# Optimization experiments

Hardware: AMD Instinct MI355X
Metric: run time of the kernel (lower is better)

The kernel has to match this reference:

```python
import jax, jax.numpy as jnp
import numpy as np

EPS = 0.1

def _kernels():
    # torch: sobel = [[-0.5,0,0.5]]*3 (2D), repeated along depth -> [1,1,3,3,3]
    s = np.array([[-0.5, 0.0, 0.5]] * 3, dtype=np.float32)        # grad along W
    kx = np.tile(s[None, :, :], (3, 1, 1))                        # [3,3,3]
    ky = np.tile(s.T[None, :, :], (3, 1, 1))                      # grad along H
    kz = np.zeros((3, 3, 3), dtype=np.float32)
    kz[0, :, :] = -0.5
    kz[2, :, :] = 0.5                                             # grad along D
    # OIDHW, O=I=1 (channel=1 depthwise)
    return (jnp.asarray(kx)[None, None], jnp.asarray(ky)[None, None], jnp.asarray(kz)[None, None])

KX, KY, KZ = _kernels()

def _conv(x, k):
    return jax.lax.conv_general_dilated(
        x, k, window_strides=(1, 1, 1), padding='VALID',
        dimension_numbers=('NCDHW', 'OIDHW', 'NCDHW'))

def _grads(x):
    # ReplicationPad3d(1) == edge padding on D,H,W
    xp = jnp.pad(x, ((0, 0), (0, 0), (1, 1), (1, 1), (1, 1)), mode='edge')
    return _conv(xp, KX), _conv(xp, KY), _conv(xp, KZ)

def setup_inputs() -> dict:
    key = jax.random.key(0)
    k1, k2, k3 = jax.random.split(key, 3)
    shp = (1, 1, 192, 192, 192)
    return {
        'I': jax.random.normal(k1, shp, dtype=jnp.float32),
        'J': jax.random.normal(k2, shp, dtype=jnp.float32),
        'mask': jax.random.uniform(k3, shp, dtype=jnp.float32),
    }

def reference(I, J, mask):
    Ix, Iy, Iz = _grads(I)
    Jx, Jy, Jz = _grads(J)
    I_mag = Ix * Ix + Iy * Iy + Iz * Iz + EPS * EPS
    J_mag = Jx * Jx + Jy * Jy + Jz * Jz + EPS * EPS
    dot = Ix * Jx + Iy * Jy + Iz * Jz          # == sum over concat channel dim (C=1)
    ngf = (dot * dot) / (I_mag * J_mag)
    return jnp.mean((1.0 - ngf) * mask)
```

## Files before the change

### kernel.cpp

```cpp
#include <hip/hip_runtime.h>

#define NN 192
#define BZ 4
#define YC 12
#define NTHR (64 * BZ)


__device__ __forceinline__ void fold_pq(const float3 rm, const float3 r0, const float3 rp,
                                        int lane, float pe[5], float qe[5]) {
    const float p0 = rm.x + r0.x + rp.x;
    const float p1 = rm.y + r0.y + rp.y;
    const float p2 = rm.z + r0.z + rp.z;
    const float q0 = rp.x - rm.x;
    const float q1 = rp.y - rm.y;
    const float q2 = rp.z - rm.z;
    float pL = __shfl_up(p2, 1, 64);
    float pR = __shfl_down(p0, 1, 64);
    float qL = __shfl_up(q2, 1, 64);
    float qR = __shfl_down(q0, 1, 64);
    if (lane == 0)  { pL = p0; qL = q0; }
    if (lane == 63) { pR = p2; qR = q2; }
    pe[0] = pL; pe[1] = p0; pe[2] = p1; pe[3] = p2; pe[4] = pR;
    qe[0] = qL; qe[1] = q0; qe[2] = q1; qe[3] = q2; qe[4] = qR;
}

__device__ __forceinline__ void load_plane(const float* const base[6], int yrow,
                                           float3 rI[3], float3 rJ[3]) {
#pragma unroll
    for (int d = 0; d < 3; ++d) rI[d] = *reinterpret_cast<const float3*>(base[d] + yrow);
#pragma unroll
    for (int d = 0; d < 3; ++d) rJ[d] = *reinterpret_cast<const float3*>(base[3 + d] + yrow);
}

__global__ __launch_bounds__(NTHR, 3) void ngf_kernel(const float* __restrict__ I,
                                                      const float* __restrict__ J,
                                                      const float* __restrict__ M,
                                                      float* __restrict__ out) {
    const int lane = threadIdx.x;
    const int tz = threadIdx.y;
    const int xoff = lane * 3;
    const int z = blockIdx.y * BZ + tz;
    const int ybase = blockIdx.x * YC;

    const int gzm = (z == 0) ? 0 : z - 1;
    const int gzp = (z == NN - 1) ? (NN - 1) : z + 1;

    const float* base[6] = {
        I + gzm * NN * NN + xoff, I + z * NN * NN + xoff, I + gzp * NN * NN + xoff,
        J + gzm * NN * NN + xoff, J + z * NN * NN + xoff, J + gzp * NN * NN + xoff};
    const float* mbase = M + z * NN * NN + xoff;

    float pe[2][3][5], qe[2][3][5];

    {
        float3 rI[3], rJ[3];
        load_plane(base, ((ybase == 0) ? 0 : (ybase - 1)) * NN, rI, rJ);
        fold_pq(rI[0], rI[1], rI[2], lane, pe[0][0], qe[0][0]);
        fold_pq(rJ[0], rJ[1], rJ[2], lane, pe[1][0], qe[1][0]);
        load_plane(base, ybase * NN, rI, rJ);
        fold_pq(rI[0], rI[1], rI[2], lane, pe[0][1], qe[0][1]);
        fold_pq(rJ[0], rJ[1], rJ[2], lane, pe[1][1], qe[1][1]);
    }

    float3 bI[2][3], bJ[2][3];
    load_plane(base, (ybase + 1) * NN, bI[0], bJ[0]);
    float3 mcur = *reinterpret_cast<const float3*>(mbase + ybase * NN);

    float acc = 0.0f;
#pragma unroll
    for (int yy = 0; yy < YC; ++yy) {
        const int cb = yy & 1, nb = cb ^ 1;

        float3 mnxt = mcur;
        if (yy < YC - 1) {
            int gy = ybase + yy + 2;
            gy = (gy > NN - 1) ? (NN - 1) : gy;
            load_plane(base, gy * NN, bI[nb], bJ[nb]);
            mnxt = *reinterpret_cast<const float3*>(mbase + (ybase + yy + 1) * NN);
        }

        const int sC = (yy + 2) % 3;
        fold_pq(bI[cb][0], bI[cb][1], bI[cb][2], lane, pe[0][sC], qe[0][sC]);
        fold_pq(bJ[cb][0], bJ[cb][1], bJ[cb][2], lane, pe[1][sC], qe[1][sC]);

        const int s0 = yy % 3, s1 = (yy + 1) % 3;
        float G[2][3][3];
#pragma unroll
        for (int ar = 0; ar < 2; ++ar) {
            float S[5], D[5], T[5];
#pragma unroll
            for (int i = 0; i < 5; ++i) {
                S[i] = pe[ar][s0][i] + pe[ar][s1][i] + pe[ar][sC][i];
                D[i] = pe[ar][sC][i] - pe[ar][s0][i];
                T[i] = qe[ar][s0][i] + qe[ar][s1][i] + qe[ar][sC][i];
            }
#pragma unroll
            for (int i = 0; i < 3; ++i) {
                G[ar][0][i] = S[i + 2] - S[i];
                G[ar][1][i] = D[i] + D[i + 1] + D[i + 2];
                G[ar][2][i] = T[i] + T[i + 1] + T[i + 2];
            }
        }
        const float mm[3] = {mcur.x, mcur.y, mcur.z};
#pragma unroll
        for (int i = 0; i < 3; ++i) {
            const float Ix = G[0][0][i], Iy = G[0][1][i], Iz = G[0][2][i];
            const float Jx = G[1][0][i], Jy = G[1][1][i], Jz = G[1][2][i];
            const float im = Ix * Ix + Iy * Iy + Iz * Iz + 0.04f;
            const float jm = Jx * Jx + Jy * Jy + Jz * Jz + 0.04f;
            const float dot = Ix * Jx + Iy * Jy + Iz * Jz;
            acc += (1.0f - dot * dot * __builtin_amdgcn_rcpf(im * jm)) * mm[i];
        }
        mcur = mnxt;
    }

    acc *= (1.0f / ((float)NN * (float)NN * (float)NN));
#pragma unroll
    for (int off = 32; off > 0; off >>= 1)
        acc += __shfl_down(acc, off, 64);

    __shared__ float red[NTHR / 64];
    const int flat = tz * 64 + lane;
    if ((flat & 63) == 0) red[flat >> 6] = acc;
    __syncthreads();
    if (flat == 0) {
        float s = 0.0f;
#pragma unroll
        for (int w = 0; w < NTHR / 64; ++w) s += red[w];
        atomicAdd(out, s);
    }
}

extern "C" void kernel_launch(void* const* d_in, const int* in_sizes, int n_in,
                              void* d_out, int out_size, void* d_ws, size_t ws_size,
                              hipStream_t stream) {
    const float* I = (const float*)d_in[0];
    const float* J = (const float*)d_in[1];
    const float* M = (const float*)d_in[2];
    float* out = (float*)d_out;

    hipMemsetAsync(d_out, 0, sizeof(float), stream);

    dim3 block(64, BZ);
    dim3 grid(NN / YC, NN / BZ);
    ngf_kernel<<<grid, block, 0, stream>>>(I, J, M, out);
}
```

Measured before the change: 121.7 us.

## Share z-neighbor rows across warps via double-buffered LDS staging

Each block now loads the six distinct z-planes (BZ+2) for I and J once per y-row into shared memory, instead of every warp loading its own three z-planes from global memory. Warps then read their stencil neighbors from LDS through a double buffer, with one barrier per row. This cuts redundant global/L2 traffic by roughly half. In exchange it adds a __syncthreads per iteration and LDS usage, and it changes YC from 12 to 8 and the launch bound to 4 blocks per SM.

```diff
diff --git a/kernel.cpp b/kernel.cpp
--- a/kernel.cpp
+++ b/kernel.cpp
@@ -2,8 +2,11 @@
 
 #define NN 192
 #define BZ 4
-#define YC 12
-#define NTHR (64 * BZ)
+#define YC 8
+#define NTHR 256
+#define ROWF 192
+#define ROWS 12
+#define BUF_F (ROWS * ROWF)
 
 
 __device__ __forceinline__ void fold_pq(const float3 rm, const float3 r0, const float3 rp,
@@ -24,66 +27,94 @@
     qe[0] = qL; qe[1] = q0; qe[2] = q1; qe[3] = q2; qe[4] = qR;
 }
 
-__device__ __forceinline__ void load_plane(const float* const base[6], int yrow,
-                                           float3 rI[3], float3 rJ[3]) {
-#pragma unroll
-    for (int d = 0; d < 3; ++d) rI[d] = *reinterpret_cast<const float3*>(base[d] + yrow);
-#pragma unroll
-    for (int d = 0; d < 3; ++d) rJ[d] = *reinterpret_cast<const float3*>(base[3 + d] + yrow);
-}
-
-__global__ __launch_bounds__(NTHR, 3) void ngf_kernel(const float* __restrict__ I,
+__global__ __launch_bounds__(NTHR, 4) void ngf_kernel(const float* __restrict__ I,
                                                       const float* __restrict__ J,
                                                       const float* __restrict__ M,
                                                       float* __restrict__ out) {
+    __shared__ float sbuf[2 * BUF_F];
+    __shared__ float red[NTHR / 64];
+
     const int lane = threadIdx.x;
     const int tz = threadIdx.y;
-    const int xoff = lane * 3;
-    const int z = blockIdx.y * BZ + tz;
+    const int z0 = blockIdx.y * BZ;
+    const int z = z0 + tz;
     const int ybase = blockIdx.x * YC;
 
-    const int gzm = (z == 0) ? 0 : z - 1;
-    const int gzp = (z == NN - 1) ? (NN - 1) : z + 1;
-
-    const float* base[6] = {
-        I + gzm * NN * NN + xoff, I + z * NN * NN + xoff, I + gzp * NN * NN + xoff,
-        J + gzm * NN * NN + xoff, J + z * NN * NN + xoff, J + gzp * NN * NN + xoff};
-    const float* mbase = M + z * NN * NN + xoff;
+    const float* srow[3];
+    int loff[3];
+#pragma unroll
+    for (int j = 0; j < 3; ++j) {
+        const int rr = tz * 3 + j;
+        const int arr = rr / 6;
+        const int zr = rr - arr * 6;
+        int zc = z0 - 1 + zr;
+        zc = zc < 0 ? 0 : (zc > NN - 1 ? NN - 1 : zc);
+        srow[j] = (arr ? J : I) + zc * NN * NN + lane * 3;
+        loff[j] = rr * ROWF + lane * 3;
+    }
+    const float* mbase = M + z * NN * NN + lane * 3;
 
     float pe[2][3][5], qe[2][3][5];
+    float3 R[3];
 
     {
-        float3 rI[3], rJ[3];
-        load_plane(base, ((ybase == 0) ? 0 : (ybase - 1)) * NN, rI, rJ);
-        fold_pq(rI[0], rI[1], rI[2], lane, pe[0][0], qe[0][0]);
-        fold_pq(rJ[0], rJ[1], rJ[2], lane, pe[1][0], qe[1][0]);
-        load_plane(base, ybase * NN, rI, rJ);
-        fold_pq(rI[0], rI[1], rI[2], lane, pe[0][1], qe[0][1]);
-        fold_pq(rJ[0], rJ[1], rJ[2], lane, pe[1][1], qe[1][1]);
+        const int gy = (ybase == 0) ? 0 : (ybase - 1);
+#pragma unroll
+        for (int j = 0; j < 3; ++j) R[j] = *(const float3*)(srow[j] + gy * NN);
+#pragma unroll
+        for (int j = 0; j < 3; ++j) *(float3*)&sbuf[0 * BUF_F + loff[j]] = R[j];
+        __syncthreads();
+#pragma unroll
+        for (int ar = 0; ar < 2; ++ar) {
+            const float* bb = sbuf + 0 * BUF_F + (ar * 6 + tz) * ROWF + lane * 3;
+            fold_pq(*(const float3*)(bb), *(const float3*)(bb + ROWF),
+                    *(const float3*)(bb + 2 * ROWF), lane, pe[ar][0], qe[ar][0]);
+        }
     }
-
-    float3 bI[2][3], bJ[2][3];
-    load_plane(base, (ybase + 1) * NN, bI[0], bJ[0]);
-    float3 mcur = *reinterpret_cast<const float3*>(mbase + ybase * NN);
+    {
+#pragma unroll
+        for (int j = 0; j < 3; ++j) R[j] = *(const float3*)(srow[j] + ybase * NN);
+#pragma unroll
+        for (int j = 0; j < 3; ++j) *(float3*)&sbuf[1 * BUF_F + loff[j]] = R[j];
+        __syncthreads();
+#pragma unroll
+        for (int ar = 0; ar < 2; ++ar) {
+            const float* bb = sbuf + 1 * BUF_F + (ar * 6 + tz) * ROWF + lane * 3;
+            fold_pq(*(const float3*)(bb), *(const float3*)(bb + ROWF),
+                    *(const float3*)(bb + 2 * ROWF), lane, pe[ar][1], qe[ar][1]);
+        }
+    }
+#pragma unroll
+    for (int j = 0; j < 3; ++j) R[j] = *(const float3*)(srow[j] + (ybase + 1) * NN);
+    float3 mcur = *(const float3*)(mbase + ybase * NN);
 
     float acc = 0.0f;
 #pragma unroll
     for (int yy = 0; yy < YC; ++yy) {
-        const int cb = yy & 1, nb = cb ^ 1;
+        const int bw = yy & 1;
+        const int sC = (yy + 2) % 3;
+        const int s0 = yy % 3, s1 = (yy + 1) % 3;
+
+#pragma unroll
+        for (int j = 0; j < 3; ++j) *(float3*)&sbuf[bw * BUF_F + loff[j]] = R[j];
+        __syncthreads();
 
         float3 mnxt = mcur;
         if (yy < YC - 1) {
             int gy = ybase + yy + 2;
             gy = (gy > NN - 1) ? (NN - 1) : gy;
-            load_plane(base, gy * NN, bI[nb], bJ[nb]);
-            mnxt = *reinterpret_cast<const float3*>(mbase + (ybase + yy + 1) * NN);
+#pragma unroll
+            for (int j = 0; j < 3; ++j) R[j] = *(const float3*)(srow[j] + gy * NN);
+            mnxt = *(const float3*)(mbase + (ybase + yy + 1) * NN);
         }
 
-        const int sC = (yy + 2) % 3;
-        fold_pq(bI[cb][0], bI[cb][1], bI[cb][2], lane, pe[0][sC], qe[0][sC]);
-        fold_pq(bJ[cb][0], bJ[cb][1], bJ[cb][2], lane, pe[1][sC], qe[1][sC]);
+#pragma unroll
+        for (int ar = 0; ar < 2; ++ar) {
+            const float* bb = sbuf + bw * BUF_F + (ar * 6 + tz) * ROWF + lane * 3;
+            fold_pq(*(const float3*)(bb), *(const float3*)(bb + ROWF),
+                    *(const float3*)(bb + 2 * ROWF), lane, pe[ar][sC], qe[ar][sC]);
+        }
 
-        const int s0 = yy % 3, s1 = (yy + 1) % 3;
         float G[2][3][3];
 #pragma unroll
         for (int ar = 0; ar < 2; ++ar) {
@@ -119,11 +150,9 @@
     for (int off = 32; off > 0; off >>= 1)
         acc += __shfl_down(acc, off, 64);
 
-    __shared__ float red[NTHR / 64];
-    const int flat = tz * 64 + lane;
-    if ((flat & 63) == 0) red[flat >> 6] = acc;
+    if (lane == 0) red[tz] = acc;
     __syncthreads();
-    if (flat == 0) {
+    if (tz == 0 && lane == 0) {
         float s = 0.0f;
 #pragma unroll
         for (int w = 0; w < NTHR / 64; ++w) s += red[w];
```

Result: no change. 122.8 us (+0.9%).
